# Kernel tuning notes

Hardware: AMD Instinct MI355X
Metric: run time of the kernel (lower is better)

Reference implementation:

```python
import jax, jax.numpy as jnp
import numpy as np
from jax import lax

KERNEL_SIZE = 3
DILATION = 1
STRIDE = 1


def setup_inputs() -> dict:
    key = jax.random.key(0)
    k1, k2, k3, k4 = jax.random.split(key, 4)
    B, C_in, L = 8, 256, 4096
    C_out = 256
    out_len = L - DILATION * (KERNEL_SIZE - 1)  # 4094, 'valid' conv
    x = jax.random.normal(k1, (B, C_in, L), dtype=jnp.float32)
    offsets = jax.random.normal(k2, (B, 1, out_len, KERNEL_SIZE), dtype=jnp.float32)
    fan_in = C_in * KERNEL_SIZE
    weight = jax.random.normal(k3, (C_out, C_in, KERNEL_SIZE), dtype=jnp.float32) / np.sqrt(fan_in)
    bias = jax.random.normal(k4, (C_out,), dtype=jnp.float32) / np.sqrt(fan_in)
    return {"x": x, "offsets": offsets, "weight": weight, "bias": bias}


def reference(x, offsets, weight, bias):
    # x: [B, C, L]; offsets: [B, 1, out_len, K]; weight: [C_out, C, K]
    B, C, L = x.shape
    out_len = offsets.shape[-2]
    K = weight.shape[-1]
    dtype = x.dtype

    # dilated kernel sample positions: linspace(0, dilation*(K-1), K)
    dil_pos = (jnp.arange(K, dtype=dtype) * DILATION)  # [K]
    t0s = (jnp.arange(out_len, dtype=dtype) * STRIDE)[:, None]  # [out_len, 1]

    # continuous sample locations, constrained to [t0, t0 + max(dil_pos)]
    T = t0s + dil_pos + offsets  # [B, 1, out_len, K]
    T = jnp.clip(T, t0s, t0s + dil_pos[-1])

    # integer neighbors (indices are non-differentiable)
    U0 = lax.stop_gradient(
        jnp.clip(jnp.floor(T), 0, L - 2).astype(jnp.int32)
    )  # [B, 1, out_len, K]
    U1 = U0 + 1

    def gather(idx):
        # idx: [B, 1, out_len, K] -> gather along L, broadcast over channels
        flat = jnp.broadcast_to(idx.reshape(B, 1, out_len * K), (B, C, out_len * K))
        return jnp.take_along_axis(x, flat, axis=2).reshape(B, C, out_len, K)

    x0 = gather(U0)
    x1 = gather(U1)

    # linear-interpolation weights (tent kernel), broadcast [B,1,out_len,K]
    w0 = jnp.maximum(0.0, 1.0 - jnp.abs(U0.astype(dtype) - T))
    w1 = jnp.maximum(0.0, 1.0 - jnp.abs(U1.astype(dtype) - T))

    interp = w0 * x0 + w1 * x1  # [B, C, out_len, K]

    # conv1d(flatten(interp), weight, stride=K) == per-position K-tap contraction
    out = jnp.einsum("bctk,ock->bot", interp, weight) + bias[None, :, None]
    return out  # [B, C_out, out_len]
```

## Files before the change

### kernel.cpp

```cpp
#include <hip/hip_runtime.h>
#include <stdint.h>


constexpr int CIN  = 256;
constexpr int LX   = 4096;
constexpr int KT   = 3;
constexpr int OUTL = 4094;
constexpr int COUT = 256;
constexpr int BN   = 64;
constexpr int WPOS = 68;
constexpr int NQ   = 24;
constexpr int EPIW = 68;

typedef __attribute__((ext_vector_type(8))) short bf16x8;
typedef __attribute__((ext_vector_type(4))) float f32x4;
typedef __attribute__((ext_vector_type(16))) float f32x16;

__device__ __forceinline__ short f2bf(float f) {
  union { float f; uint32_t u; } v; v.f = f;
  return (short)((v.u + 0x8000u) >> 16);
}
__device__ __forceinline__ float bf2f(short s) {
  union { uint32_t u; float f; } v;
  v.u = ((uint32_t)(uint16_t)s) << 16;
  return v.f;
}

__global__ __launch_bounds__(256) void pack_weights_kernel(
    const float* __restrict__ w, short* __restrict__ ap) {
  const int gid = blockIdx.x * 256 + threadIdx.x;
  if (gid >= NQ * 2 * 8 * 64) return;
  const int l   = gid & 63;
  const int mf  = (gid >> 6) & 7;
  const int h   = (gid >> 9) & 1;
  const int q   = gid >> 10;
  const int ch  = q / 12;
  const int ks  = q % 12;
  const int tap = ks >> 2;
  const int c0  = ch * 128 + (ks & 3) * 32 + h * 16 + (l >> 5) * 8;
  const int row = mf * 32 + (l & 31);
  bf16x8 v;
  #pragma unroll
  for (int j = 0; j < 8; ++j) {
    v[j] = f2bf(w[((size_t)row * CIN + c0 + j) * KT + tap]);
  }
  *(bf16x8*)(ap + (size_t)gid * 8) = v;
}

__global__ __launch_bounds__(512, 4) void deform_gemm_kernel(
    const float* __restrict__ x, const float* __restrict__ off,
    const short* __restrict__ ap, const float* __restrict__ bias,
    float* __restrict__ out) {

  __shared__ __align__(16) char smem[17408 + 16384 + 1024];
  short* Xt    = (short*)smem;
  short* Bp    = (short*)(smem + 17408);
  float* Epi   = (float*)smem;
  float* biasS = (float*)(smem + 17408 + 16384);

  const int tid  = threadIdx.x;
  const int lane = tid & 63;
  const int wid  = tid >> 6;
  const int l31  = lane & 31;
  const int lh   = lane >> 5;

  const int b    = blockIdx.x & 7;
  const int rest = blockIdx.x >> 3;
  const int th   = rest & 1;
  const int tt   = rest >> 1;
  const int t0   = tt * 128 + th * 64;

  float w0m[3], w1m[3];
  int   d0m[3];
  {
    const int t = t0 + (tid & 63);
    #pragma unroll
    for (int k = 0; k < KT; ++k) {
      float w0 = 0.f, w1 = 0.f; int d0 = 0;
      if (t < OUTL) {
        const float o = off[((size_t)b * OUTL + t) * KT + k];
        float T = (float)(t + k) + o;
        T = fminf(fmaxf(T, (float)t), (float)(t + 2));
        int U0 = (int)T;
        if (U0 > LX - 2) U0 = LX - 2;
        w1 = T - (float)U0;
        w0 = 1.f - w1;
        d0 = U0 - t0;
      }
      w0m[k] = w0; w1m[k] = w1; d0m[k] = d0;
    }
  }
  if (tid < COUT) biasS[tid] = bias[tid];

  f32x16 acc0 = {0.f,0.f,0.f,0.f,0.f,0.f,0.f,0.f,0.f,0.f,0.f,0.f,0.f,0.f,0.f,0.f};
  f32x16 acc1 = {0.f,0.f,0.f,0.f,0.f,0.f,0.f,0.f,0.f,0.f,0.f,0.f,0.f,0.f,0.f,0.f};

  const float* xb = x + (size_t)b * CIN * LX;

  const short* apw = ap + wid * 512 + lane * 8;
  bf16x8 aC0 = *(const bf16x8*)apw;
  bf16x8 aC1 = *(const bf16x8*)(apw + 4096);

  #pragma unroll 1
  for (int ch = 0; ch < 2; ++ch) {
    if (ch) __syncthreads();
    #pragma unroll 1
    for (int rep = 0; rep < 17; ++rep) {
      const int idx = rep * 512 + tid;
      const int c   = idx / WPOS;
      const int pos = idx - c * WPOS;
      const int l   = t0 + pos;
      const float f = (l < LX) ? xb[(size_t)(ch * 128 + c) * LX + l] : 0.f;
      const int wi  = (pos * 128 + c) ^ ((pos & 7) << 3);
      Xt[wi] = f2bf(f);
    }
    __syncthreads();

    #pragma unroll
    for (int tap = 0; tap < KT; ++tap) {
      if (tap) __syncthreads();

      {
        const int tq = tid & 63;
        const int c0 = (tid >> 6) * 16;
        const float w0 = w0m[tap], w1 = w1m[tap];
        const int   d0 = d0m[tap];
        const int sw0 = (d0 & 7) << 3;
        const int sw1 = ((d0 + 1) & 7) << 3;
        const int r0i = d0 * 128, r1i = (d0 + 1) * 128;
        const bf16x8 r0a = *(const bf16x8*)&Xt[(r0i + c0)     ^ sw0];
        const bf16x8 r0b = *(const bf16x8*)&Xt[(r0i + c0 + 8) ^ sw0];
        const bf16x8 r1a = *(const bf16x8*)&Xt[(r1i + c0)     ^ sw1];
        const bf16x8 r1b = *(const bf16x8*)&Xt[(r1i + c0 + 8) ^ sw1];
        bf16x8 o1, o2;
        #pragma unroll
        for (int j = 0; j < 8; ++j) {
          o1[j] = f2bf(bf2f(r0a[j]) * w0 + bf2f(r1a[j]) * w1);
          o2[j] = f2bf(bf2f(r0b[j]) * w0 + bf2f(r1b[j]) * w1);
        }
        const int swt = (tq & 7) << 3;
        *(bf16x8*)&Bp[(tq * 128 + c0)     ^ swt] = o1;
        *(bf16x8*)&Bp[(tq * 128 + c0 + 8) ^ swt] = o2;
      }
      __syncthreads();

      #pragma unroll 1
      for (int csub = 0; csub < 4; ++csub) {
        const int q  = ch * 12 + tap * 4 + csub;
        const int qn = q < NQ - 1 ? q + 1 : NQ - 1;
        const bf16x8 aN0 = *(const bf16x8*)(apw + (size_t)qn * 8192);
        const bf16x8 aN1 = *(const bf16x8*)(apw + (size_t)qn * 8192 + 4096);

        const int cbase = csub * 32 + lh * 8;
        const int ta = l31,      swa = (ta & 7) << 3;
        const int tb = 32 + l31, swb = (tb & 7) << 3;
        const bf16x8 b00 = *(const bf16x8*)&Bp[(ta * 128 + cbase)      ^ swa];
        const bf16x8 b01 = *(const bf16x8*)&Bp[(ta * 128 + cbase + 16) ^ swa];
        const bf16x8 b10 = *(const bf16x8*)&Bp[(tb * 128 + cbase)      ^ swb];
        const bf16x8 b11 = *(const bf16x8*)&Bp[(tb * 128 + cbase + 16) ^ swb];

        acc0 = __builtin_amdgcn_mfma_f32_32x32x16_bf16(aC0, b00, acc0, 0, 0, 0);
        acc0 = __builtin_amdgcn_mfma_f32_32x32x16_bf16(aC1, b01, acc0, 0, 0, 0);
        acc1 = __builtin_amdgcn_mfma_f32_32x32x16_bf16(aC0, b10, acc1, 0, 0, 0);
        acc1 = __builtin_amdgcn_mfma_f32_32x32x16_bf16(aC1, b11, acc1, 0, 0, 0);

        aC0 = aN0; aC1 = aN1;
      }
    }
  }

  const size_t obase = (size_t)b * COUT * OUTL;
  #pragma unroll
  for (int p = 0; p < 4; ++p) {
    __syncthreads();
    if ((wid >> 1) == p) {
      const int lrb = (wid & 1) * 32;
      #pragma unroll
      for (int r = 0; r < 16; ++r) {
        const int rowl = (r & 3) + 8 * (r >> 2) + 4 * lh;
        const int grow = p * 64 + lrb + rowl;
        Epi[(lrb + rowl) * EPIW + l31]      = acc0[r] + biasS[grow];
        Epi[(lrb + rowl) * EPIW + 32 + l31] = acc1[r] + biasS[grow];
      }
    }
    __syncthreads();
    const int rr = tid >> 3;
    const int c8 = (tid & 7) * 8;
    float* op = out + obase + (size_t)(p * 64 + rr) * OUTL + t0 + c8;
    const f32x4 v0 = *(const f32x4*)&Epi[rr * EPIW + c8];
    const f32x4 v1 = *(const f32x4*)&Epi[rr * EPIW + c8 + 4];
    if (t0 + c8 + 7 < OUTL) {
      *(f32x4*)op = v0;
      *(f32x4*)(op + 4) = v1;
    } else {
      #pragma unroll
      for (int e = 0; e < 4; ++e) {
        if (t0 + c8 + e < OUTL)     op[e]     = v0[e];
        if (t0 + c8 + 4 + e < OUTL) op[4 + e] = v1[e];
      }
    }
  }
}

extern "C" void kernel_launch(void* const* d_in, const int* in_sizes, int n_in,
                              void* d_out, int out_size, void* d_ws, size_t ws_size,
                              hipStream_t stream) {
  const float* x    = (const float*)d_in[0];
  const float* off  = (const float*)d_in[1];
  const float* wgt  = (const float*)d_in[2];
  const float* bias = (const float*)d_in[3];
  float* out  = (float*)d_out;
  short* ap   = (short*)d_ws;

  pack_weights_kernel<<<dim3(NQ * 2 * 8 * 64 / 256), dim3(256), 0, stream>>>(wgt, ap);
  deform_gemm_kernel<<<dim3(512), dim3(512), 0, stream>>>(x, off, ap, bias, out);
}
```

Baseline: 48.09 us.

## Double-buffer input tile and prefetch second channel half with float4 loads

Replaces the scalar per-element global loads of x with float4 vector loads. Channel-half 0 is staged into its own LDS buffer up front, while the loads for channel-half 1 are issued early into registers and written to a second LDS buffer after the first half's MMAs finish. The goal is to hide global-load latency behind compute and cut load instruction count. In exchange it uses more LDS and holds 20 extra live floats in registers, which under the existing 512x4 launch bound could cause spills.

```diff
diff --git a/kernel.cpp b/kernel.cpp
--- a/kernel.cpp
+++ b/kernel.cpp
@@ -7,10 +7,10 @@
 constexpr int KT   = 3;
 constexpr int OUTL = 4094;
 constexpr int COUT = 256;
-constexpr int BN   = 64;
 constexpr int WPOS = 68;
 constexpr int NQ   = 24;
 constexpr int EPIW = 68;
+constexpr int NIT  = 2176;
 
 typedef __attribute__((ext_vector_type(8))) short bf16x8;
 typedef __attribute__((ext_vector_type(4))) float f32x4;
@@ -24,6 +24,14 @@
   union { uint32_t u; float f; } v;
   v.u = ((uint32_t)(uint16_t)s) << 16;
   return v.f;
+}
+__device__ __forceinline__ float4 loadx4(const float* p, int l) {
+  if (l + 3 < LX) return *(const float4*)(p + l);
+  float4 v; v.x = v.y = v.z = v.w = 0.f;
+  if (l + 0 < LX) v.x = p[l + 0];
+  if (l + 1 < LX) v.y = p[l + 1];
+  if (l + 2 < LX) v.z = p[l + 2];
+  return v;
 }
 
 __global__ __launch_bounds__(256) void pack_weights_kernel(
@@ -52,11 +60,12 @@
     const short* __restrict__ ap, const float* __restrict__ bias,
     float* __restrict__ out) {
 
-  __shared__ __align__(16) char smem[17408 + 16384 + 1024];
-  short* Xt    = (short*)smem;
-  short* Bp    = (short*)(smem + 17408);
+  __shared__ __align__(16) char smem[2 * 17408 + 16384 + 1024];
+  short* Xt0   = (short*)smem;
+  short* Xt1   = (short*)(smem + 17408);
+  short* Bp    = (short*)(smem + 34816);
   float* Epi   = (float*)smem;
-  float* biasS = (float*)(smem + 17408 + 16384);
+  float* biasS = (float*)(smem + 51200);
 
   const int tid  = threadIdx.x;
   const int lane = tid & 63;
@@ -69,6 +78,14 @@
   const int th   = rest & 1;
   const int tt   = rest >> 1;
   const int t0   = tt * 128 + th * 64;
+
+  int xc[5], xg[5];
+  #pragma unroll
+  for (int r = 0; r < 5; ++r) {
+    const int idx = r * 512 + tid;
+    xc[r] = idx / 17;
+    xg[r] = idx - xc[r] * 17;
+  }
 
   float w0m[3], w1m[3];
   int   d0m[3];
@@ -101,25 +118,34 @@
   bf16x8 aC0 = *(const bf16x8*)apw;
   bf16x8 aC1 = *(const bf16x8*)(apw + 4096);
 
+  float4 xv[5];
+  #pragma unroll
+  for (int r = 0; r < 5; ++r)
+    if (r * 512 + tid < NIT) xv[r] = loadx4(xb + (size_t)xc[r] * LX, t0 + 4 * xg[r]);
+  #pragma unroll
+  for (int r = 0; r < 5; ++r)
+    if (r * 512 + tid < NIT) {
+      const float fe[4] = {xv[r].x, xv[r].y, xv[r].z, xv[r].w};
+      #pragma unroll
+      for (int e = 0; e < 4; ++e) {
+        const int pos = xg[r] * 4 + e;
+        Xt0[(pos * 128 + xc[r]) ^ ((pos & 7) << 3)] = f2bf(fe[e]);
+      }
+    }
+  __syncthreads();
+
+  #pragma unroll
+  for (int r = 0; r < 5; ++r)
+    if (r * 512 + tid < NIT)
+      xv[r] = loadx4(xb + (size_t)(128 + xc[r]) * LX, t0 + 4 * xg[r]);
+
   #pragma unroll 1
   for (int ch = 0; ch < 2; ++ch) {
-    if (ch) __syncthreads();
-    #pragma unroll 1
-    for (int rep = 0; rep < 17; ++rep) {
-      const int idx = rep * 512 + tid;
-      const int c   = idx / WPOS;
-      const int pos = idx - c * WPOS;
-      const int l   = t0 + pos;
-      const float f = (l < LX) ? xb[(size_t)(ch * 128 + c) * LX + l] : 0.f;
-      const int wi  = (pos * 128 + c) ^ ((pos & 7) << 3);
-      Xt[wi] = f2bf(f);
-    }
-    __syncthreads();
+    short* Xc = ch ? Xt1 : Xt0;
 
     #pragma unroll
     for (int tap = 0; tap < KT; ++tap) {
-      if (tap) __syncthreads();
-
+      if (tap | ch) __syncthreads();
       {
         const int tq = tid & 63;
         const int c0 = (tid >> 6) * 16;
@@ -128,10 +154,10 @@
         const int sw0 = (d0 & 7) << 3;
         const int sw1 = ((d0 + 1) & 7) << 3;
         const int r0i = d0 * 128, r1i = (d0 + 1) * 128;
-        const bf16x8 r0a = *(const bf16x8*)&Xt[(r0i + c0)     ^ sw0];
-        const bf16x8 r0b = *(const bf16x8*)&Xt[(r0i + c0 + 8) ^ sw0];
-        const bf16x8 r1a = *(const bf16x8*)&Xt[(r1i + c0)     ^ sw1];
-        const bf16x8 r1b = *(const bf16x8*)&Xt[(r1i + c0 + 8) ^ sw1];
+        const bf16x8 r0a = *(const bf16x8*)&Xc[(r0i + c0)     ^ sw0];
+        const bf16x8 r0b = *(const bf16x8*)&Xc[(r0i + c0 + 8) ^ sw0];
+        const bf16x8 r1a = *(const bf16x8*)&Xc[(r1i + c0)     ^ sw1];
+        const bf16x8 r1b = *(const bf16x8*)&Xc[(r1i + c0 + 8) ^ sw1];
         bf16x8 o1, o2;
         #pragma unroll
         for (int j = 0; j < 8; ++j) {
@@ -166,6 +192,19 @@
 
         aC0 = aN0; aC1 = aN1;
       }
+    }
+
+    if (ch == 0) {
+      #pragma unroll
+      for (int r = 0; r < 5; ++r)
+        if (r * 512 + tid < NIT) {
+          const float fe[4] = {xv[r].x, xv[r].y, xv[r].z, xv[r].w};
+          #pragma unroll
+          for (int e = 0; e < 4; ++e) {
+            const int pos = xg[r] * 4 + e;
+            Xt1[(pos * 128 + xc[r]) ^ ((pos & 7) << 3)] = f2bf(fe[e]);
+          }
+        }
     }
   }
 
```

Result: faster. 44.10 us (-8.3%).

## Halve position tile to 32 and vectorize x staging loads

Applied to the files above, without the earlier changes.

Shrinks each block's output-position tile from 64 to 32 and launches twice as many blocks, each warp now doing one MFMA accumulator instead of two, with smaller LDS and a higher occupancy hint. The x staging loop switches from scalar strided loads to float4 loads and then scatters them into the swizzled bf16 tile. The aim is more blocks across the CUs and fewer global load instructions. In exchange the weight fragments are loaded twice as often overall and the halo overhead grows relative to the tile (36 staged positions for 32 outputs).

```diff
diff --git a/kernel.cpp b/kernel.cpp
--- a/kernel.cpp
+++ b/kernel.cpp
@@ -7,10 +7,11 @@
 constexpr int KT   = 3;
 constexpr int OUTL = 4094;
 constexpr int COUT = 256;
-constexpr int BN   = 64;
-constexpr int WPOS = 68;
+constexpr int BN   = 32;
+constexpr int WPOS = 36;
 constexpr int NQ   = 24;
-constexpr int EPIW = 68;
+constexpr int EPIW = 36;
+constexpr int NIT  = 1152;
 
 typedef __attribute__((ext_vector_type(8))) short bf16x8;
 typedef __attribute__((ext_vector_type(4))) float f32x4;
@@ -24,6 +25,14 @@
   union { uint32_t u; float f; } v;
   v.u = ((uint32_t)(uint16_t)s) << 16;
   return v.f;
+}
+__device__ __forceinline__ float4 loadx4(const float* p, int l) {
+  if (l + 3 < LX) return *(const float4*)(p + l);
+  float4 v; v.x = v.y = v.z = v.w = 0.f;
+  if (l + 0 < LX) v.x = p[l + 0];
+  if (l + 1 < LX) v.y = p[l + 1];
+  if (l + 2 < LX) v.z = p[l + 2];
+  return v;
 }
 
 __global__ __launch_bounds__(256) void pack_weights_kernel(
@@ -47,16 +56,16 @@
   *(bf16x8*)(ap + (size_t)gid * 8) = v;
 }
 
-__global__ __launch_bounds__(512, 4) void deform_gemm_kernel(
+__global__ __launch_bounds__(512, 6) void deform_gemm_kernel(
     const float* __restrict__ x, const float* __restrict__ off,
     const short* __restrict__ ap, const float* __restrict__ bias,
     float* __restrict__ out) {
 
-  __shared__ __align__(16) char smem[17408 + 16384 + 1024];
+  __shared__ __align__(16) char smem[9216 + 8192 + 1024];
   short* Xt    = (short*)smem;
-  short* Bp    = (short*)(smem + 17408);
+  short* Bp    = (short*)(smem + 9216);
   float* Epi   = (float*)smem;
-  float* biasS = (float*)(smem + 17408 + 16384);
+  float* biasS = (float*)(smem + 9216 + 8192);
 
   const int tid  = threadIdx.x;
   const int lane = tid & 63;
@@ -64,16 +73,14 @@
   const int l31  = lane & 31;
   const int lh   = lane >> 5;
 
-  const int b    = blockIdx.x & 7;
-  const int rest = blockIdx.x >> 3;
-  const int th   = rest & 1;
-  const int tt   = rest >> 1;
-  const int t0   = tt * 128 + th * 64;
+  const int b  = blockIdx.x & 7;
+  const int tt = blockIdx.x >> 3;
+  const int t0 = tt * BN;
 
   float w0m[3], w1m[3];
   int   d0m[3];
   {
-    const int t = t0 + (tid & 63);
+    const int t = t0 + (tid & 31);
     #pragma unroll
     for (int k = 0; k < KT; ++k) {
       float w0 = 0.f, w1 = 0.f; int d0 = 0;
@@ -92,8 +99,7 @@
   }
   if (tid < COUT) biasS[tid] = bias[tid];
 
-  f32x16 acc0 = {0.f,0.f,0.f,0.f,0.f,0.f,0.f,0.f,0.f,0.f,0.f,0.f,0.f,0.f,0.f,0.f};
-  f32x16 acc1 = {0.f,0.f,0.f,0.f,0.f,0.f,0.f,0.f,0.f,0.f,0.f,0.f,0.f,0.f,0.f,0.f};
+  f32x16 acc = {0.f,0.f,0.f,0.f,0.f,0.f,0.f,0.f,0.f,0.f,0.f,0.f,0.f,0.f,0.f,0.f};
 
   const float* xb = x + (size_t)b * CIN * LX;
 
@@ -104,15 +110,29 @@
   #pragma unroll 1
   for (int ch = 0; ch < 2; ++ch) {
     if (ch) __syncthreads();
-    #pragma unroll 1
-    for (int rep = 0; rep < 17; ++rep) {
-      const int idx = rep * 512 + tid;
-      const int c   = idx / WPOS;
-      const int pos = idx - c * WPOS;
-      const int l   = t0 + pos;
-      const float f = (l < LX) ? xb[(size_t)(ch * 128 + c) * LX + l] : 0.f;
-      const int wi  = (pos * 128 + c) ^ ((pos & 7) << 3);
-      Xt[wi] = f2bf(f);
+    {
+      float4 xv[3];
+      #pragma unroll
+      for (int r = 0; r < 3; ++r) {
+        const int idx = r * 512 + tid;
+        if (idx < NIT) {
+          const int c = idx / 9, g = idx - c * 9;
+          xv[r] = loadx4(xb + (size_t)(ch * 128 + c) * LX, t0 + 4 * g);
+        }
+      }
+      #pragma unroll
+      for (int r = 0; r < 3; ++r) {
+        const int idx = r * 512 + tid;
+        if (idx < NIT) {
+          const int c = idx / 9, g = idx - c * 9;
+          const float fe[4] = {xv[r].x, xv[r].y, xv[r].z, xv[r].w};
+          #pragma unroll
+          for (int e = 0; e < 4; ++e) {
+            const int pos = g * 4 + e;
+            Xt[(pos * 128 + c) ^ ((pos & 7) << 3)] = f2bf(fe[e]);
+          }
+        }
+      }
     }
     __syncthreads();
 
@@ -121,26 +141,19 @@
       if (tap) __syncthreads();
 
       {
-        const int tq = tid & 63;
-        const int c0 = (tid >> 6) * 16;
+        const int tq = tid & 31;
+        const int c0 = (tid >> 5) * 8;
         const float w0 = w0m[tap], w1 = w1m[tap];
         const int   d0 = d0m[tap];
         const int sw0 = (d0 & 7) << 3;
         const int sw1 = ((d0 + 1) & 7) << 3;
-        const int r0i = d0 * 128, r1i = (d0 + 1) * 128;
-        const bf16x8 r0a = *(const bf16x8*)&Xt[(r0i + c0)     ^ sw0];
-        const bf16x8 r0b = *(const bf16x8*)&Xt[(r0i + c0 + 8) ^ sw0];
-        const bf16x8 r1a = *(const bf16x8*)&Xt[(r1i + c0)     ^ sw1];
-        const bf16x8 r1b = *(const bf16x8*)&Xt[(r1i + c0 + 8) ^ sw1];
-        bf16x8 o1, o2;
+        const bf16x8 r0 = *(const bf16x8*)&Xt[(d0 * 128 + c0)       ^ sw0];
+        const bf16x8 r1 = *(const bf16x8*)&Xt[((d0 + 1) * 128 + c0) ^ sw1];
+        bf16x8 o;
         #pragma unroll
-        for (int j = 0; j < 8; ++j) {
-          o1[j] = f2bf(bf2f(r0a[j]) * w0 + bf2f(r1a[j]) * w1);
-          o2[j] = f2bf(bf2f(r0b[j]) * w0 + bf2f(r1b[j]) * w1);
-        }
-        const int swt = (tq & 7) << 3;
-        *(bf16x8*)&Bp[(tq * 128 + c0)     ^ swt] = o1;
-        *(bf16x8*)&Bp[(tq * 128 + c0 + 8) ^ swt] = o2;
+        for (int j = 0; j < 8; ++j)
+          o[j] = f2bf(bf2f(r0[j]) * w0 + bf2f(r1[j]) * w1);
+        *(bf16x8*)&Bp[(tq * 128 + c0) ^ ((tq & 7) << 3)] = o;
       }
       __syncthreads();
 
@@ -152,17 +165,12 @@
         const bf16x8 aN1 = *(const bf16x8*)(apw + (size_t)qn * 8192 + 4096);
 
         const int cbase = csub * 32 + lh * 8;
-        const int ta = l31,      swa = (ta & 7) << 3;
-        const int tb = 32 + l31, swb = (tb & 7) << 3;
-        const bf16x8 b00 = *(const bf16x8*)&Bp[(ta * 128 + cbase)      ^ swa];
-        const bf16x8 b01 = *(const bf16x8*)&Bp[(ta * 128 + cbase + 16) ^ swa];
-        const bf16x8 b10 = *(const bf16x8*)&Bp[(tb * 128 + cbase)      ^ swb];
-        const bf16x8 b11 = *(const bf16x8*)&Bp[(tb * 128 + cbase + 16) ^ swb];
-
-        acc0 = __builtin_amdgcn_mfma_f32_32x32x16_bf16(aC0, b00, acc0, 0, 0, 0);
-        acc0 = __builtin_amdgcn_mfma_f32_32x32x16_bf16(aC1, b01, acc0, 0, 0, 0);
-        acc1 = __builtin_amdgcn_mfma_f32_32x32x16_bf16(aC0, b10, acc1, 0, 0, 0);
-        acc1 = __builtin_amdgcn_mfma_f32_32x32x16_bf16(aC1, b11, acc1, 0, 0, 0);
+        const int swt   = (l31 & 7) << 3;
+        const bf16x8 b0 = *(const bf16x8*)&Bp[(l31 * 128 + cbase)      ^ swt];
+        const bf16x8 b1 = *(const bf16x8*)&Bp[(l31 * 128 + cbase + 16) ^ swt];
+
+        acc = __builtin_amdgcn_mfma_f32_32x32x16_bf16(aC0, b0, acc, 0, 0, 0);
+        acc = __builtin_amdgcn_mfma_f32_32x32x16_bf16(aC1, b1, acc, 0, 0, 0);
 
         aC0 = aN0; aC1 = aN1;
       }
@@ -178,26 +186,21 @@
       #pragma unroll
       for (int r = 0; r < 16; ++r) {
         const int rowl = (r & 3) + 8 * (r >> 2) + 4 * lh;
-        const int grow = p * 64 + lrb + rowl;
-        Epi[(lrb + rowl) * EPIW + l31]      = acc0[r] + biasS[grow];
-        Epi[(lrb + rowl) * EPIW + 32 + l31] = acc1[r] + biasS[grow];
+        Epi[(lrb + rowl) * EPIW + l31] = acc[r] + biasS[wid * 32 + rowl];
       }
     }
     __syncthreads();
     const int rr = tid >> 3;
-    const int c8 = (tid & 7) * 8;
-    float* op = out + obase + (size_t)(p * 64 + rr) * OUTL + t0 + c8;
-    const f32x4 v0 = *(const f32x4*)&Epi[rr * EPIW + c8];
-    const f32x4 v1 = *(const f32x4*)&Epi[rr * EPIW + c8 + 4];
-    if (t0 + c8 + 7 < OUTL) {
-      *(f32x4*)op = v0;
-      *(f32x4*)(op + 4) = v1;
+    const int c4 = (tid & 7) * 4;
+    const f32x4 v = *(const f32x4*)&Epi[rr * EPIW + c4];
+    const int   t = t0 + c4;
+    float* op = out + obase + (size_t)(p * 64 + rr) * OUTL + t;
+    if (t + 3 < OUTL) {
+      *(f32x4*)op = v;
     } else {
       #pragma unroll
-      for (int e = 0; e < 4; ++e) {
-        if (t0 + c8 + e < OUTL)     op[e]     = v0[e];
-        if (t0 + c8 + 4 + e < OUTL) op[4 + e] = v1[e];
-      }
+      for (int e = 0; e < 4; ++e)
+        if (t + e < OUTL) op[e] = v[e];
     }
   }
 }
@@ -213,5 +216,5 @@
   short* ap   = (short*)d_ws;
 
   pack_weights_kernel<<<dim3(NQ * 2 * 8 * 64 / 256), dim3(256), 0, stream>>>(wgt, ap);
-  deform_gemm_kernel<<<dim3(512), dim3(512), 0, stream>>>(x, off, ap, bias, out);
-}
+  deform_gemm_kernel<<<dim3(1024), dim3(512), 0, stream>>>(x, off, ap, bias, out);
+}
```

After: 68.14 us. +41.7%, slower.

## Stage x tile in fp32 channel-major LDS with float4 global loads

Applied to the files above, without the earlier changes.

The x tile moves from a position-major, swizzled bf16 layout filled by scalar strided loads to a channel-major fp32 layout filled by float4 vector loads. Global reads become coalesced and wide, and the interpolation skips a bf16 round trip on x. In exchange the interpolation step now does 32 scalar LDS reads per thread in place of four 16-byte reads, and the staging buffer doubles in size, which may reduce occupancy. The MFMA B-fragment loads are also reordered and interleaved with the MFMAs.

```diff
diff --git a/kernel.cpp b/kernel.cpp
--- a/kernel.cpp
+++ b/kernel.cpp
@@ -7,10 +7,10 @@
 constexpr int KT   = 3;
 constexpr int OUTL = 4094;
 constexpr int COUT = 256;
-constexpr int BN   = 64;
 constexpr int WPOS = 68;
 constexpr int NQ   = 24;
 constexpr int EPIW = 68;
+constexpr int NIT  = 2176;
 
 typedef __attribute__((ext_vector_type(8))) short bf16x8;
 typedef __attribute__((ext_vector_type(4))) float f32x4;
@@ -20,10 +20,13 @@
   union { float f; uint32_t u; } v; v.f = f;
   return (short)((v.u + 0x8000u) >> 16);
 }
-__device__ __forceinline__ float bf2f(short s) {
-  union { uint32_t u; float f; } v;
-  v.u = ((uint32_t)(uint16_t)s) << 16;
-  return v.f;
+__device__ __forceinline__ float4 loadx4(const float* p, int l) {
+  if (l + 3 < LX) return *(const float4*)(p + l);
+  float4 v; v.x = v.y = v.z = v.w = 0.f;
+  if (l + 0 < LX) v.x = p[l + 0];
+  if (l + 1 < LX) v.y = p[l + 1];
+  if (l + 2 < LX) v.z = p[l + 2];
+  return v;
 }
 
 __global__ __launch_bounds__(256) void pack_weights_kernel(
@@ -52,11 +55,11 @@
     const short* __restrict__ ap, const float* __restrict__ bias,
     float* __restrict__ out) {
 
-  __shared__ __align__(16) char smem[17408 + 16384 + 1024];
-  short* Xt    = (short*)smem;
-  short* Bp    = (short*)(smem + 17408);
+  __shared__ __align__(16) char smem[34816 + 16384 + 1024];
+  float* Xs    = (float*)smem;
+  short* Bp    = (short*)(smem + 34816);
   float* Epi   = (float*)smem;
-  float* biasS = (float*)(smem + 17408 + 16384);
+  float* biasS = (float*)(smem + 51200);
 
   const int tid  = threadIdx.x;
   const int lane = tid & 63;
@@ -104,15 +107,14 @@
   #pragma unroll 1
   for (int ch = 0; ch < 2; ++ch) {
     if (ch) __syncthreads();
-    #pragma unroll 1
-    for (int rep = 0; rep < 17; ++rep) {
-      const int idx = rep * 512 + tid;
-      const int c   = idx / WPOS;
-      const int pos = idx - c * WPOS;
-      const int l   = t0 + pos;
-      const float f = (l < LX) ? xb[(size_t)(ch * 128 + c) * LX + l] : 0.f;
-      const int wi  = (pos * 128 + c) ^ ((pos & 7) << 3);
-      Xt[wi] = f2bf(f);
+    #pragma unroll
+    for (int r = 0; r < 5; ++r) {
+      const int idx = r * 512 + tid;
+      if (idx < NIT) {
+        const int c = idx / 17, g = idx - c * 17;
+        const float4 v = loadx4(xb + (size_t)(ch * 128 + c) * LX, t0 + 4 * g);
+        *(float4*)&Xs[c * WPOS + 4 * g] = v;
+      }
     }
     __syncthreads();
 
@@ -122,25 +124,25 @@
 
       {
         const int tq = tid & 63;
-        const int c0 = (tid >> 6) * 16;
+        const int cb = (tid >> 6) * 16;
         const float w0 = w0m[tap], w1 = w1m[tap];
         const int   d0 = d0m[tap];
-        const int sw0 = (d0 & 7) << 3;
-        const int sw1 = ((d0 + 1) & 7) << 3;
-        const int r0i = d0 * 128, r1i = (d0 + 1) * 128;
-        const bf16x8 r0a = *(const bf16x8*)&Xt[(r0i + c0)     ^ sw0];
-        const bf16x8 r0b = *(const bf16x8*)&Xt[(r0i + c0 + 8) ^ sw0];
-        const bf16x8 r1a = *(const bf16x8*)&Xt[(r1i + c0)     ^ sw1];
-        const bf16x8 r1b = *(const bf16x8*)&Xt[(r1i + c0 + 8) ^ sw1];
+        const int swt = (tq & 7) << 3;
         bf16x8 o1, o2;
         #pragma unroll
         for (int j = 0; j < 8; ++j) {
-          o1[j] = f2bf(bf2f(r0a[j]) * w0 + bf2f(r1a[j]) * w1);
-          o2[j] = f2bf(bf2f(r0b[j]) * w0 + bf2f(r1b[j]) * w1);
-        }
-        const int swt = (tq & 7) << 3;
-        *(bf16x8*)&Bp[(tq * 128 + c0)     ^ swt] = o1;
-        *(bf16x8*)&Bp[(tq * 128 + c0 + 8) ^ swt] = o2;
+          const float xa0 = Xs[(cb + j) * WPOS + d0];
+          const float xa1 = Xs[(cb + j) * WPOS + d0 + 1];
+          o1[j] = f2bf(xa0 * w0 + xa1 * w1);
+        }
+        *(bf16x8*)&Bp[(tq * 128 + cb) ^ swt] = o1;
+        #pragma unroll
+        for (int j = 0; j < 8; ++j) {
+          const float xb0 = Xs[(cb + 8 + j) * WPOS + d0];
+          const float xb1 = Xs[(cb + 8 + j) * WPOS + d0 + 1];
+          o2[j] = f2bf(xb0 * w0 + xb1 * w1);
+        }
+        *(bf16x8*)&Bp[(tq * 128 + cb + 8) ^ swt] = o2;
       }
       __syncthreads();
 
@@ -154,16 +156,18 @@
         const int cbase = csub * 32 + lh * 8;
         const int ta = l31,      swa = (ta & 7) << 3;
         const int tb = 32 + l31, swb = (tb & 7) << 3;
-        const bf16x8 b00 = *(const bf16x8*)&Bp[(ta * 128 + cbase)      ^ swa];
-        const bf16x8 b01 = *(const bf16x8*)&Bp[(ta * 128 + cbase + 16) ^ swa];
-        const bf16x8 b10 = *(const bf16x8*)&Bp[(tb * 128 + cbase)      ^ swb];
-        const bf16x8 b11 = *(const bf16x8*)&Bp[(tb * 128 + cbase + 16) ^ swb];
-
-        acc0 = __builtin_amdgcn_mfma_f32_32x32x16_bf16(aC0, b00, acc0, 0, 0, 0);
-        acc0 = __builtin_amdgcn_mfma_f32_32x32x16_bf16(aC1, b01, acc0, 0, 0, 0);
-        acc1 = __builtin_amdgcn_mfma_f32_32x32x16_bf16(aC0, b10, acc1, 0, 0, 0);
-        acc1 = __builtin_amdgcn_mfma_f32_32x32x16_bf16(aC1, b11, acc1, 0, 0, 0);
-
+        {
+          const bf16x8 b00 = *(const bf16x8*)&Bp[(ta * 128 + cbase) ^ swa];
+          const bf16x8 b10 = *(const bf16x8*)&Bp[(tb * 128 + cbase) ^ swb];
+          acc0 = __builtin_amdgcn_mfma_f32_32x32x16_bf16(aC0, b00, acc0, 0, 0, 0);
+          acc1 = __builtin_amdgcn_mfma_f32_32x32x16_bf16(aC0, b10, acc1, 0, 0, 0);
+        }
+        {
+          const bf16x8 b01 = *(const bf16x8*)&Bp[(ta * 128 + cbase + 16) ^ swa];
+          const bf16x8 b11 = *(const bf16x8*)&Bp[(tb * 128 + cbase + 16) ^ swb];
+          acc0 = __builtin_amdgcn_mfma_f32_32x32x16_bf16(aC1, b01, acc0, 0, 0, 0);
+          acc1 = __builtin_amdgcn_mfma_f32_32x32x16_bf16(aC1, b11, acc1, 0, 0, 0);
+        }
         aC0 = aN0; aC1 = aN1;
       }
     }
```

New measurement: 40.39 us. -16.0%, faster.
